# Optimization experiments

Hardware: AMD Instinct MI355X
Metric: run time of the kernel (lower is better)

The kernel has to match this reference:

```python
import jax, jax.numpy as jnp
import numpy as np

K = 7  # kernel_size
C, H, W = 32, 192, 192


def setup_inputs() -> dict:
    key = jax.random.key(0)
    k1, k2, k3, k4 = jax.random.split(key, 4)
    x = jax.random.normal(k1, (C, H, W, 2), dtype=jnp.float32)
    # per-pixel kernel: (1, 1, K^2, H, W); original inits to ones/K^2, randomize for testing
    weight1 = jax.random.normal(k2, (1, 1, K * K, H, W), dtype=jnp.float32) / (K * K)
    # 1x1 conv c->c: weight (C_out, C_in) and bias (C,)
    conv_w = jax.random.normal(k3, (C, C), dtype=jnp.float32) / np.sqrt(C).astype(np.float32)
    conv_b = jax.random.normal(k4, (C,), dtype=jnp.float32) * 0.01
    return {"x": x, "weight1": weight1, "conv_w": conv_w, "conv_b": conv_b}


def conv_pixelwise(x, kernel):
    # x: (n, c, h, w); kernel: (1, 1, K^2, h, w)
    # Equivalent to: pad, unfold(K), reshape (n,c,K^2,h,w), * kernel, sum over K^2.
    # Implemented as a fused shift-multiply-accumulate over the K^2 fixed taps
    p = K // 2
    n, c, h, w = x.shape
    xp = jnp.pad(x, ((0, 0), (0, 0), (p, p), (p, p)))
    out = jnp.zeros_like(x)
    for i in range(K):
        for j in range(K):
            # F.unfold ordering: row-major over the KxK window -> index i*K + j
            out = out + xp[:, :, i:i + h, j:j + w] * kernel[:, :, i * K + j]
    return out


def reference(x, weight1, conv_w, conv_b):
    # x: (c, h, w, 2) -> (2, c, h, w)
    xi = jnp.transpose(x, (3, 0, 1, 2))
    xi = conv_pixelwise(xi, weight1)
    # 1x1 conv over channels + bias
    xi = jnp.einsum('nchw,oc->nohw', xi, conv_w) + conv_b[None, :, None, None]
    # back to (c, h, w, 2)
    return jnp.transpose(xi, (1, 2, 3, 0))
```

## Files before the change

kernel.cpp:

```cpp
#include <hip/hip_runtime.h>

#define C 32
#define H 192
#define W 192
#define HW (H*W)
#define NPIX (HW*2)
#define KK 7
#define TAPS 49

__global__ __launch_bounds__(256) void k1_mix(
    const float* __restrict__ x, const float* __restrict__ cw, float* __restrict__ z)
{
    __shared__ float wl[256];
    const int b  = blockIdx.x;
    const int l  = (b & 7) * 72 + (b >> 3);
    const int hwblk = l >> 2;
    const int ob    = (l & 3) * 8;
    const int tid   = threadIdx.x;

    wl[tid] = cw[(ob + (tid & 7)) * C + (tid >> 3)];
    __syncthreads();

    const int hw = hwblk * 256 + tid;
    const float2* x2 = reinterpret_cast<const float2*>(x);
    float2 xv[C];
#pragma unroll
    for (int c = 0; c < C; ++c) xv[c] = x2[(size_t)c * HW + hw];

    float acc[8][2];
#pragma unroll
    for (int oo = 0; oo < 8; ++oo) { acc[oo][0] = 0.f; acc[oo][1] = 0.f; }

#pragma unroll
    for (int c = 0; c < C; ++c) {
        const float4 wa = *reinterpret_cast<const float4*>(&wl[c * 8]);
        const float4 wb = *reinterpret_cast<const float4*>(&wl[c * 8 + 4]);
        const float wt[8] = { wa.x, wa.y, wa.z, wa.w, wb.x, wb.y, wb.z, wb.w };
#pragma unroll
        for (int oo = 0; oo < 8; ++oo) {
            acc[oo][0] += wt[oo] * xv[c].x;
            acc[oo][1] += wt[oo] * xv[c].y;
        }
    }

    float* zp = z + (size_t)hw * 64 + ob * 2;
#pragma unroll
    for (int q = 0; q < 4; ++q) {
        float4 r = make_float4(acc[2*q][0], acc[2*q][1], acc[2*q+1][0], acc[2*q+1][1]);
        *reinterpret_cast<float4*>(zp + 4 * q) = r;
    }
}

#define K2_BLOCKS 1152
__global__ __launch_bounds__(256) void k2_conv(
    const float* __restrict__ z, const float* __restrict__ w1,
    const float* __restrict__ cb, float* __restrict__ out)
{
    __shared__ float wl[TAPS * 32];
    __shared__ float tr[4][8 * 66];

    const int b  = blockIdx.x;
    const int l  = (b & 7) * (K2_BLOCKS / 8) + (b >> 3);
    const int h  = l / 6;
    const int wq = l % 6;
    const int tid  = threadIdx.x;
    const int wv   = tid >> 6;
    const int lane = tid & 63;
    const int w0   = wq * 32 + wv * 8;

#pragma unroll
    for (int k = 0; k < 7; ++k) {
        const int v = k * 256 + tid;
        if (v < TAPS * 32) {
            const int t = v >> 5, c = v & 31;
            wl[v] = w1[(size_t)t * HW + h * W + wq * 32 + c];
        }
    }
    __syncthreads();

    float acc[8];
#pragma unroll
    for (int p = 0; p < 8; ++p) acc[p] = 0.f;

#pragma unroll
    for (int i = 0; i < KK; ++i) {
        const int yy = h + i - 3;
        if (yy < 0 || yy >= H) continue;

        float zw[14];
        const float* zr = z + (size_t)yy * (W * 64) + lane;
#pragma unroll
        for (int k = 0; k < 14; ++k) {
            const int cc  = w0 - 3 + k;
            const int ccc = cc < 0 ? 0 : (cc > W - 1 ? W - 1 : cc);
            const float v = zr[ccc * 64];
            zw[k] = (cc == ccc) ? v : 0.f;
        }

#pragma unroll
        for (int j = 0; j < KK; ++j) {
            const float4 wa = *reinterpret_cast<const float4*>(&wl[(i*KK + j) * 32 + wv * 8]);
            const float4 wb4 = *reinterpret_cast<const float4*>(&wl[(i*KK + j) * 32 + wv * 8 + 4]);
            acc[0] += wa.x  * zw[j + 0];
            acc[1] += wa.y  * zw[j + 1];
            acc[2] += wa.z  * zw[j + 2];
            acc[3] += wa.w  * zw[j + 3];
            acc[4] += wb4.x * zw[j + 4];
            acc[5] += wb4.y * zw[j + 5];
            acc[6] += wb4.z * zw[j + 6];
            acc[7] += wb4.w * zw[j + 7];
        }
    }

    const float bias = cb[lane >> 1];
    float* trw = &tr[wv][0];
#pragma unroll
    for (int p = 0; p < 8; ++p) trw[p * 66 + lane] = acc[p] + bias;
    __syncthreads();

    const int o = lane >> 1, half = lane & 1;
    float v8[8];
#pragma unroll
    for (int m = 0; m < 8; ++m) {
        const int f = half * 8 + m;
        v8[m] = trw[(f >> 1) * 66 + o * 2 + (f & 1)];
    }
    float* obase = out + (size_t)o * NPIX + ((size_t)h * W + w0) * 2 + half * 8;
    *reinterpret_cast<float4*>(obase)     = make_float4(v8[0], v8[1], v8[2], v8[3]);
    *reinterpret_cast<float4*>(obase + 4) = make_float4(v8[4], v8[5], v8[6], v8[7]);
}

extern "C" void kernel_launch(void* const* d_in, const int* in_sizes, int n_in,
                              void* d_out, int out_size, void* d_ws, size_t ws_size,
                              hipStream_t stream) {
    const float* x  = (const float*)d_in[0];
    const float* w1 = (const float*)d_in[1];
    const float* cw = (const float*)d_in[2];
    const float* cb = (const float*)d_in[3];
    float* z   = (float*)d_ws;
    float* out = (float*)d_out;

    hipLaunchKernelGGL(k1_mix, dim3(576), dim3(256), 0, stream, x, cw, z);
    hipLaunchKernelGGL(k2_conv, dim3(K2_BLOCKS), dim3(256), 0, stream, z, w1, cb, out);
}
```

Measured before the change: 25.51 us.

## Specialize edge cases and software-pipeline z row loads; read per-pixel weights directly

Removes the shared-memory staging of per-pixel tap weights and its block barrier, so each wave reads its weights straight from global memory as wave-uniform scalar loads. The row loop is split into template specializations for interior and edge tiles, so interior tiles skip clamping and masking. Up to four rows of z are held in registers ahead of the FMAs to overlap load latency with compute. The cost is higher register pressure and four code-path variants, plus repeated global weight reads in place of a single shared copy.

Result: slower. 28.39 us (+11.3%).

```diff
diff --git a/kernel.cpp b/kernel.cpp
--- a/kernel.cpp
+++ b/kernel.cpp
@@ -6,7 +6,6 @@
 #define HW (H*W)
 #define NPIX (HW*2)
 #define KK 7
-#define TAPS 49
 
 __global__ __launch_bounds__(256) void k1_mix(
     const float* __restrict__ x, const float* __restrict__ cw, float* __restrict__ z)
@@ -52,65 +51,87 @@
 }
 
 #define K2_BLOCKS 1152
+
+template<bool WEDGE>
+__device__ __forceinline__ void load_row(const float* __restrict__ z, int yy, int w0,
+                                         int lane, float* buf)
+{
+    if (!WEDGE) {
+        const float* p = z + ((size_t)yy * W + (w0 - 3)) * 64 + lane;
+#pragma unroll
+        for (int k = 0; k < 14; ++k) buf[k] = p[k * 64];
+    } else {
+        const float* p = z + (size_t)yy * W * 64 + lane;
+#pragma unroll
+        for (int k = 0; k < 14; ++k) {
+            const int cc  = w0 - 3 + k;
+            const int ccl = cc < 0 ? 0 : (cc > W - 1 ? W - 1 : cc);
+            const float v = p[ccl * 64];
+            buf[k] = (cc == ccl) ? v : 0.f;
+        }
+    }
+}
+
+__device__ __forceinline__ void fma_row(const float* __restrict__ w1, int i, int h, int w0,
+                                        const float* buf, float* acc)
+{
+    const float* wp = w1 + (size_t)i * KK * HW + (size_t)h * W + w0;
+#pragma unroll
+    for (int j = 0; j < KK; ++j) {
+#pragma unroll
+        for (int px = 0; px < 8; ++px)
+            acc[px] += wp[j * HW + px] * buf[j + px];
+    }
+}
+
+template<bool WEDGE, bool HEDGE>
+__device__ __forceinline__ void k2_body(const float* __restrict__ z, const float* __restrict__ w1,
+                                        int h, int w0, int lane, float* acc)
+{
+    float b0[14], b1[14], b2[14], b3[14];
+    auto LR = [&](float* buf, int i) {
+        const int yy = h + i - 3;
+        if (HEDGE && ((unsigned)yy >= (unsigned)H)) {
+#pragma unroll
+            for (int k = 0; k < 14; ++k) buf[k] = 0.f;
+        } else {
+            load_row<WEDGE>(z, yy, w0, lane, buf);
+        }
+    };
+    LR(b0, 0); LR(b1, 1); LR(b2, 2); LR(b3, 3);
+    fma_row(w1, 0, h, w0, b0, acc); LR(b0, 4);
+    fma_row(w1, 1, h, w0, b1, acc); LR(b1, 5);
+    fma_row(w1, 2, h, w0, b2, acc); LR(b2, 6);
+    fma_row(w1, 3, h, w0, b3, acc);
+    fma_row(w1, 4, h, w0, b0, acc);
+    fma_row(w1, 5, h, w0, b1, acc);
+    fma_row(w1, 6, h, w0, b2, acc);
+}
+
 __global__ __launch_bounds__(256) void k2_conv(
     const float* __restrict__ z, const float* __restrict__ w1,
     const float* __restrict__ cb, float* __restrict__ out)
 {
-    __shared__ float wl[TAPS * 32];
     __shared__ float tr[4][8 * 66];
 
     const int b  = blockIdx.x;
     const int l  = (b & 7) * (K2_BLOCKS / 8) + (b >> 3);
     const int h  = l / 6;
     const int wq = l % 6;
-    const int tid  = threadIdx.x;
-    const int wv   = tid >> 6;
-    const int lane = tid & 63;
+    const int wv   = __builtin_amdgcn_readfirstlane(threadIdx.x >> 6);
+    const int lane = threadIdx.x & 63;
     const int w0   = wq * 32 + wv * 8;
-
-#pragma unroll
-    for (int k = 0; k < 7; ++k) {
-        const int v = k * 256 + tid;
-        if (v < TAPS * 32) {
-            const int t = v >> 5, c = v & 31;
-            wl[v] = w1[(size_t)t * HW + h * W + wq * 32 + c];
-        }
-    }
-    __syncthreads();
 
     float acc[8];
 #pragma unroll
     for (int p = 0; p < 8; ++p) acc[p] = 0.f;
 
-#pragma unroll
-    for (int i = 0; i < KK; ++i) {
-        const int yy = h + i - 3;
-        if (yy < 0 || yy >= H) continue;
-
-        float zw[14];
-        const float* zr = z + (size_t)yy * (W * 64) + lane;
-#pragma unroll
-        for (int k = 0; k < 14; ++k) {
-            const int cc  = w0 - 3 + k;
-            const int ccc = cc < 0 ? 0 : (cc > W - 1 ? W - 1 : cc);
-            const float v = zr[ccc * 64];
-            zw[k] = (cc == ccc) ? v : 0.f;
-        }
-
-#pragma unroll
-        for (int j = 0; j < KK; ++j) {
-            const float4 wa = *reinterpret_cast<const float4*>(&wl[(i*KK + j) * 32 + wv * 8]);
-            const float4 wb4 = *reinterpret_cast<const float4*>(&wl[(i*KK + j) * 32 + wv * 8 + 4]);
-            acc[0] += wa.x  * zw[j + 0];
-            acc[1] += wa.y  * zw[j + 1];
-            acc[2] += wa.z  * zw[j + 2];
-            acc[3] += wa.w  * zw[j + 3];
-            acc[4] += wb4.x * zw[j + 4];
-            acc[5] += wb4.y * zw[j + 5];
-            acc[6] += wb4.z * zw[j + 6];
-            acc[7] += wb4.w * zw[j + 7];
-        }
-    }
+    const bool wedge = (w0 == 0) || (w0 == 184);
+    const bool hedge = (h < 3) || (h > 188);
+    if (!wedge && !hedge)      k2_body<false, false>(z, w1, h, w0, lane, acc);
+    else if (!wedge && hedge)  k2_body<false, true >(z, w1, h, w0, lane, acc);
+    else if (wedge && !hedge)  k2_body<true,  false>(z, w1, h, w0, lane, acc);
+    else                       k2_body<true,  true >(z, w1, h, w0, lane, acc);
 
     const float bias = cb[lane >> 1];
     float* trw = &tr[wv][0];
```

## Split k1 output channels finer and preload all conv rows in k2

Applied to the files above, without the earlier changes.

k1 now computes 4 output channels per block instead of 8, doubling the grid to 1152 blocks to raise parallelism, at the cost of reading x twice as often. k2 issues all 7×14 z loads up front, with a fast path that skips clamping for interior columns, so memory latency overlaps instead of serializing per row. It also adds an occupancy hint of 3 blocks per CU and makes the wave index uniform via readfirstlane. Holding 98 preloaded values raises register pressure and may cause spills under the launch bound.

Measured after the change: 28.54 us. +11.9%, slower.

```diff
diff --git a/kernel.cpp b/kernel.cpp
--- a/kernel.cpp
+++ b/kernel.cpp
@@ -11,14 +11,14 @@
 __global__ __launch_bounds__(256) void k1_mix(
     const float* __restrict__ x, const float* __restrict__ cw, float* __restrict__ z)
 {
-    __shared__ float wl[256];
+    __shared__ float wl[128];
     const int b  = blockIdx.x;
-    const int l  = (b & 7) * 72 + (b >> 3);
-    const int hwblk = l >> 2;
-    const int ob    = (l & 3) * 8;
+    const int l  = (b & 7) * 144 + (b >> 3);
+    const int hwblk = l >> 3;
+    const int ob    = (l & 7) * 4;
     const int tid   = threadIdx.x;
 
-    wl[tid] = cw[(ob + (tid & 7)) * C + (tid >> 3)];
+    if (tid < 128) wl[tid] = cw[(ob + (tid & 3)) * C + (tid >> 2)];
     __syncthreads();
 
     const int hw = hwblk * 256 + tid;
@@ -27,32 +27,26 @@
 #pragma unroll
     for (int c = 0; c < C; ++c) xv[c] = x2[(size_t)c * HW + hw];
 
-    float acc[8][2];
+    float acc[4][2];
 #pragma unroll
-    for (int oo = 0; oo < 8; ++oo) { acc[oo][0] = 0.f; acc[oo][1] = 0.f; }
+    for (int oo = 0; oo < 4; ++oo) { acc[oo][0] = 0.f; acc[oo][1] = 0.f; }
 
 #pragma unroll
     for (int c = 0; c < C; ++c) {
-        const float4 wa = *reinterpret_cast<const float4*>(&wl[c * 8]);
-        const float4 wb = *reinterpret_cast<const float4*>(&wl[c * 8 + 4]);
-        const float wt[8] = { wa.x, wa.y, wa.z, wa.w, wb.x, wb.y, wb.z, wb.w };
-#pragma unroll
-        for (int oo = 0; oo < 8; ++oo) {
-            acc[oo][0] += wt[oo] * xv[c].x;
-            acc[oo][1] += wt[oo] * xv[c].y;
-        }
+        const float4 wt = *reinterpret_cast<const float4*>(&wl[c * 4]);
+        acc[0][0] += wt.x * xv[c].x;  acc[0][1] += wt.x * xv[c].y;
+        acc[1][0] += wt.y * xv[c].x;  acc[1][1] += wt.y * xv[c].y;
+        acc[2][0] += wt.z * xv[c].x;  acc[2][1] += wt.z * xv[c].y;
+        acc[3][0] += wt.w * xv[c].x;  acc[3][1] += wt.w * xv[c].y;
     }
 
     float* zp = z + (size_t)hw * 64 + ob * 2;
-#pragma unroll
-    for (int q = 0; q < 4; ++q) {
-        float4 r = make_float4(acc[2*q][0], acc[2*q][1], acc[2*q+1][0], acc[2*q+1][1]);
-        *reinterpret_cast<float4*>(zp + 4 * q) = r;
-    }
+    *reinterpret_cast<float4*>(zp)     = make_float4(acc[0][0], acc[0][1], acc[1][0], acc[1][1]);
+    *reinterpret_cast<float4*>(zp + 4) = make_float4(acc[2][0], acc[2][1], acc[3][0], acc[3][1]);
 }
 
 #define K2_BLOCKS 1152
-__global__ __launch_bounds__(256) void k2_conv(
+__global__ __launch_bounds__(256, 3) void k2_conv(
     const float* __restrict__ z, const float* __restrict__ w1,
     const float* __restrict__ cb, float* __restrict__ out)
 {
@@ -64,7 +58,7 @@
     const int h  = l / 6;
     const int wq = l % 6;
     const int tid  = threadIdx.x;
-    const int wv   = tid >> 6;
+    const int wv   = __builtin_amdgcn_readfirstlane(tid >> 6);
     const int lane = tid & 63;
     const int w0   = wq * 32 + wv * 8;
 
@@ -78,37 +72,59 @@
     }
     __syncthreads();
 
+    float zb[KK][14];
+    const bool wedge = (w0 == 0) || (w0 == W - 8);
+    if (!wedge) {
+#pragma unroll
+        for (int i = 0; i < KK; ++i) {
+            const int yy = h + i - 3;
+            if (yy >= 0 && yy < H) {
+                const float* p = z + ((size_t)yy * W + (w0 - 3)) * 64 + lane;
+#pragma unroll
+                for (int k = 0; k < 14; ++k) zb[i][k] = p[k * 64];
+            } else {
+#pragma unroll
+                for (int k = 0; k < 14; ++k) zb[i][k] = 0.f;
+            }
+        }
+    } else {
+#pragma unroll
+        for (int i = 0; i < KK; ++i) {
+            const int yy = h + i - 3;
+            if (yy >= 0 && yy < H) {
+                const float* p = z + (size_t)yy * (W * 64) + lane;
+#pragma unroll
+                for (int k = 0; k < 14; ++k) {
+                    const int cc  = w0 - 3 + k;
+                    const int ccl = cc < 0 ? 0 : (cc > W - 1 ? W - 1 : cc);
+                    const float v = p[ccl * 64];
+                    zb[i][k] = (cc == ccl) ? v : 0.f;
+                }
+            } else {
+#pragma unroll
+                for (int k = 0; k < 14; ++k) zb[i][k] = 0.f;
+            }
+        }
+    }
+
     float acc[8];
 #pragma unroll
     for (int p = 0; p < 8; ++p) acc[p] = 0.f;
 
 #pragma unroll
     for (int i = 0; i < KK; ++i) {
-        const int yy = h + i - 3;
-        if (yy < 0 || yy >= H) continue;
-
-        float zw[14];
-        const float* zr = z + (size_t)yy * (W * 64) + lane;
-#pragma unroll
-        for (int k = 0; k < 14; ++k) {
-            const int cc  = w0 - 3 + k;
-            const int ccc = cc < 0 ? 0 : (cc > W - 1 ? W - 1 : cc);
-            const float v = zr[ccc * 64];
-            zw[k] = (cc == ccc) ? v : 0.f;
-        }
-
 #pragma unroll
         for (int j = 0; j < KK; ++j) {
-            const float4 wa = *reinterpret_cast<const float4*>(&wl[(i*KK + j) * 32 + wv * 8]);
+            const float4 wa  = *reinterpret_cast<const float4*>(&wl[(i*KK + j) * 32 + wv * 8]);
             const float4 wb4 = *reinterpret_cast<const float4*>(&wl[(i*KK + j) * 32 + wv * 8 + 4]);
-            acc[0] += wa.x  * zw[j + 0];
-            acc[1] += wa.y  * zw[j + 1];
-            acc[2] += wa.z  * zw[j + 2];
-            acc[3] += wa.w  * zw[j + 3];
-            acc[4] += wb4.x * zw[j + 4];
-            acc[5] += wb4.y * zw[j + 5];
-            acc[6] += wb4.z * zw[j + 6];
-            acc[7] += wb4.w * zw[j + 7];
+            acc[0] += wa.x  * zb[i][j + 0];
+            acc[1] += wa.y  * zb[i][j + 1];
+            acc[2] += wa.z  * zb[i][j + 2];
+            acc[3] += wa.w  * zb[i][j + 3];
+            acc[4] += wb4.x * zb[i][j + 4];
+            acc[5] += wb4.y * zb[i][j + 5];
+            acc[6] += wb4.z * zb[i][j + 6];
+            acc[7] += wb4.w * zb[i][j + 7];
         }
     }
 
@@ -140,6 +156,6 @@
     float* z   = (float*)d_ws;
     float* out = (float*)d_out;
 
-    hipLaunchKernelGGL(k1_mix, dim3(576), dim3(256), 0, stream, x, cw, z);
+    hipLaunchKernelGGL(k1_mix, dim3(1152), dim3(256), 0, stream, x, cw, z);
     hipLaunchKernelGGL(k2_conv, dim3(K2_BLOCKS), dim3(256), 0, stream, z, w1, cb, out);
 }
```
